# Performance work log

Hardware: AMD Instinct MI355X
Metric: run time of the kernel (lower is better)

## Reference

```python
import jax, jax.numpy as jnp
import numpy as np

N = 40000      # nodes
E = 640000     # edges
G = 2048       # graphs
D = 128        # emb_dim
T = 10         # num_tasks
L = 5          # layers
ATOM_VOCAB = 64
BOND_VOCAB = 8
BN_EPS = 1e-5


def _bn(x, g, b, m, v):
    # inference-mode BatchNorm1d with running stats
    return (x - m) * jax.lax.rsqrt(v + BN_EPS) * g + b


def setup_inputs() -> dict:
    key = jax.random.key(0)
    ks = jax.random.split(key, 24)
    inp = {
        "x_atom": jax.random.randint(ks[0], (N, 9), 0, ATOM_VOCAB),
        "edge_index": jax.random.randint(ks[1], (2, E), 0, N),
        "edge_attr": jax.random.randint(ks[2], (E, 3), 0, BOND_VOCAB),
        "batch": jnp.sort(jax.random.randint(ks[3], (N,), 0, G)),
        # embedding tables
        "atom_emb": jax.random.normal(ks[4], (9, ATOM_VOCAB, D)) * 0.1,
        "bond_emb": jax.random.normal(ks[5], (L, 3, BOND_VOCAB, D)) * 0.1,
        # per-layer GIN params (stacked over L)
        "eps": jnp.zeros((L,)),
        "W1": jax.random.normal(ks[6], (L, D, 2 * D)) * 0.05,
        "b1": jnp.zeros((L, 2 * D)),
        "g1": jnp.ones((L, 2 * D)),
        "bt1": jnp.zeros((L, 2 * D)),
        "m1": jax.random.normal(ks[7], (L, 2 * D)) * 0.1,
        "v1": jax.random.uniform(ks[8], (L, 2 * D), minval=0.5, maxval=1.5),
        "W2": jax.random.normal(ks[9], (L, 2 * D, D)) * 0.05,
        "b2": jnp.zeros((L, D)),
        # outer BatchNorm per layer
        "gO": jnp.ones((L, D)),
        "btO": jnp.zeros((L, D)),
        "mO": jax.random.normal(ks[10], (L, D)) * 0.1,
        "vO": jax.random.uniform(ks[11], (L, D), minval=0.5, maxval=1.5),
        # prediction head
        "Wp": jax.random.normal(ks[12], (D, T)) * 0.05,
        "bp": jnp.zeros((T,)),
    }
    return inp


def reference(x_atom, edge_index, edge_attr, batch, atom_emb, bond_emb, eps,
              W1, b1, g1, bt1, m1, v1, W2, b2, gO, btO, mO, vO, Wp, bp):
    src, dst = edge_index[0], edge_index[1]
    # AtomEncoder: sum of per-feature embeddings -> [N, D]
    x = atom_emb[jnp.arange(9)[None, :], x_atom].sum(axis=1)
    feat3 = jnp.arange(3)[None, :]
    for i in range(L):
        # BondEncoder for this layer -> [E, D]
        e = bond_emb[i][feat3, edge_attr].sum(axis=1)
        # message: relu(x_j + edge_emb); aggregate: scatter-add at dst
        msg = jax.nn.relu(x[src] + e)
        agg = jax.ops.segment_sum(msg, dst, num_segments=N)
        h = (1.0 + eps[i]) * x + agg
        # MLP: Linear -> BN -> ReLU -> Linear
        h = jax.nn.relu(_bn(h @ W1[i] + b1[i], g1[i], bt1[i], m1[i], v1[i]))
        h = h @ W2[i] + b2[i]
        # outer BN; ReLU after all but last layer (dropout = identity in eval)
        x = _bn(h, gO[i], btO[i], mO[i], vO[i])
        if i < L - 1:
            x = jax.nn.relu(x)
    # global mean pool over graphs
    sums = jax.ops.segment_sum(x, batch, num_segments=G)
    cnt = jax.ops.segment_sum(jnp.ones((N,), x.dtype), batch, num_segments=G)
    pooled = sums / jnp.maximum(cnt, 1.0)[:, None]
    return pooled @ Wp + bp
```

## Files before the change

### kernel.cpp

```cpp
#include <hip/hip_runtime.h>
#include <hip/hip_bf16.h>

#define NN 40000
#define NE 640000
#define NG 2048
#define DD 128
#define NT 10
#define NL 5
#define NB 80

typedef __attribute__((ext_vector_type(8))) short short8;
typedef __attribute__((ext_vector_type(4))) float f32x4;
typedef unsigned short ushort_t;

static __device__ __forceinline__ ushort_t f2b(float f) {
    return __bfloat16_as_ushort(__float2bfloat16(f));
}
static __device__ __forceinline__ float b2f(ushort_t u) {
    return __bfloat162float(__ushort_as_bfloat16(u));
}

__global__ void __launch_bounds__(256)
k_setup(const float* __restrict__ W1, const float* __restrict__ W2,
        const float* __restrict__ bemb, const int* __restrict__ xa,
        const float* __restrict__ aemb, const int* __restrict__ ei,
        ushort_t* __restrict__ W1P, ushort_t* __restrict__ W2P,
        ushort_t* __restrict__ ebsum16, ushort_t* __restrict__ x16,
        int* __restrict__ deg) {
    int b = blockIdx.x, t = threadIdx.x;
    if (b < 1280) {
        int tid = b * 256 + t;
        int layer = tid >> 16;
        int r = tid & 65535;
        int half = r >> 15;
        int q = r & 32767;
        int j = q & 7;
        int lane = (q >> 3) & 63;
        if (half == 0) {
            int kk = (q >> 9) & 3;
            int nt = q >> 11;
            int n = nt * 16 + (lane & 15);
            int k = kk * 32 + (lane >> 4) * 8 + j;
            W1P[layer * 32768 + q] = f2b(W1[(layer * DD + k) * 256 + n]);
        } else {
            int kk = (q >> 9) & 7;
            int nt = q >> 12;
            int n = nt * 16 + (lane & 15);
            int k = kk * 32 + (lane >> 4) * 8 + j;
            W2P[layer * 32768 + q] = f2b(W2[(layer * 256 + k) * DD + n]);
        }
        int d = tid & 127;
        int c = (tid >> 7) & 511;
        const float* bl = bemb + (size_t)layer * 3 * 8 * DD;
        ebsum16[tid] = f2b(bl[(c & 7) * DD + d] + bl[(8 + ((c >> 3) & 7)) * DD + d] +
                           bl[(16 + (c >> 6)) * DD + d]);
    } else if (b < 21280) {
        int half = t >> 7, d = t & 127;
        int n = (b - 1280) * 2 + half;
        __shared__ int idx[2][9];
        if (d < 9) idx[half][d] = xa[n * 9 + d];
        __syncthreads();
        float s = 0.f;
#pragma unroll
        for (int f = 0; f < 9; ++f) s += aemb[(f * 64 + idx[half][f]) * DD + d];
        x16[n * DD + d] = f2b(s);
    } else {
        int e = (b - 21280) * 256 + t;
        atomicAdd(&deg[ei[NE + e]], 1);
    }
}


__global__ void k_scan1(const int* __restrict__ deg, int* __restrict__ off,
                        int* __restrict__ blksum) {
    int b = blockIdx.x, t = threadIdx.x;
    int i = b * 256 + t;
    __shared__ int s[256];
    int v = (i < NN) ? deg[i] : 0;
    s[t] = v;
    __syncthreads();
    for (int d = 1; d < 256; d <<= 1) {
        int add = (t >= d) ? s[t - d] : 0;
        __syncthreads();
        s[t] += add;
        __syncthreads();
    }
    if (i <= NN) off[i] = s[t] - v;
    if (t == 255) blksum[b] = s[255];
}

__global__ void k_scan2(int* __restrict__ blk) {
    int t = threadIdx.x;
    __shared__ int s[256];
    int v = blk[t];
    s[t] = v;
    __syncthreads();
    for (int d = 1; d < 256; d <<= 1) {
        int add = (t >= d) ? s[t - d] : 0;
        __syncthreads();
        s[t] += add;
        __syncthreads();
    }
    blk[256 + t] = s[t] - v;
}

__global__ void k_scan3(int* __restrict__ off, const int* __restrict__ blk) {
    int b = blockIdx.x, t = threadIdx.x;
    int i = b * 256 + t;
    if (i <= NN) off[i] += blk[256 + b];
}

__global__ void __launch_bounds__(256)
k_bucket(const int* __restrict__ ei, const int* __restrict__ ea,
         const int* __restrict__ off, int* __restrict__ gbk,
         int2* __restrict__ ebuf) {
    __shared__ int hist[NB];
    __shared__ int sbase[NB];
    int t = threadIdx.x;
    int e0 = blockIdx.x * 1024;
    if (t < NB) hist[t] = 0;
    __syncthreads();
    int rank[4], buck[4], rec[4], dstv[4];
#pragma unroll
    for (int k = 0; k < 4; ++k) {
        int e = e0 + k * 256 + t;
        int src = ei[e];
        int dst = ei[NE + e];
        int a0 = ea[e * 3 + 0], a1 = ea[e * 3 + 1], a2 = ea[e * 3 + 2];
        rec[k] = src | ((a0 | (a1 << 3) | (a2 << 6)) << 16);
        dstv[k] = dst;
        int b = dst >> 9;
        buck[k] = b;
        rank[k] = atomicAdd(&hist[b], 1);
    }
    __syncthreads();
    if (t < NB) sbase[t] = atomicAdd(&gbk[t], hist[t]);
    __syncthreads();
#pragma unroll
    for (int k = 0; k < 4; ++k) {
        int b = buck[k];
        int slot = off[b << 9] + sbase[b] + rank[k];
        ebuf[slot] = make_int2(rec[k], dstv[k]);
    }
}

__global__ void k_scatter2(const int2* __restrict__ ebuf, const int* __restrict__ off,
                           int* __restrict__ cursor, int2* __restrict__ epack) {
    int i = blockIdx.x * 256 + threadIdx.x;
    int2 s = ebuf[i];
    int dst = s.y;
    int p = off[dst] + atomicAdd(&cursor[dst], 1);
    epack[p] = make_int2(s.x & 0xFFFF, s.x >> 16);
}

__global__ void __launch_bounds__(256)
k_gather(const ushort_t* __restrict__ xin, const int* __restrict__ off,
         const int2* __restrict__ epack, const ushort_t* __restrict__ ebsum16,
         const float* __restrict__ eps, int layer, ushort_t* __restrict__ h16) {
    int t = threadIdx.x;
    int lane = t & 63;
    int n = blockIdx.x * 4 + (t >> 6);
    const ushort2* x2 = (const ushort2*)xin;
    const ushort2* eb2 = (const ushort2*)ebsum16;
    ushort2 xv = x2[n * 64 + lane];
    float es = 1.f + eps[layer];
    float ax = es * b2f(xv.x), ay = es * b2f(xv.y);
    int p = off[n], p1 = off[n + 1];

    int2 e0, e1, e2, e3;
    bool have = (p + 4 <= p1);
    if (have) { e0 = epack[p]; e1 = epack[p + 1]; e2 = epack[p + 2]; e3 = epack[p + 3]; }
    while (have) {
        int np = p + 4;
        bool nh = (np + 4 <= p1);
        int2 f0, f1, f2, f3;
        if (nh) { f0 = epack[np]; f1 = epack[np + 1]; f2 = epack[np + 2]; f3 = epack[np + 3]; }
        ushort2 v0 = eb2[e0.y * 64 + lane];
        ushort2 s0 = x2[e0.x * 64 + lane];
        ushort2 v1 = eb2[e1.y * 64 + lane];
        ushort2 s1 = x2[e1.x * 64 + lane];
        ushort2 v2 = eb2[e2.y * 64 + lane];
        ushort2 s2 = x2[e2.x * 64 + lane];
        ushort2 v3 = eb2[e3.y * 64 + lane];
        ushort2 s3 = x2[e3.x * 64 + lane];
        ax += fmaxf(b2f(v0.x) + b2f(s0.x), 0.f) + fmaxf(b2f(v1.x) + b2f(s1.x), 0.f) +
              fmaxf(b2f(v2.x) + b2f(s2.x), 0.f) + fmaxf(b2f(v3.x) + b2f(s3.x), 0.f);
        ay += fmaxf(b2f(v0.y) + b2f(s0.y), 0.f) + fmaxf(b2f(v1.y) + b2f(s1.y), 0.f) +
              fmaxf(b2f(v2.y) + b2f(s2.y), 0.f) + fmaxf(b2f(v3.y) + b2f(s3.y), 0.f);
        p = np;
        e0 = f0; e1 = f1; e2 = f2; e3 = f3;
        have = nh;
    }
    for (; p < p1; ++p) {
        int2 er = epack[p];
        ushort2 ev = eb2[er.y * 64 + lane];
        ushort2 sv = x2[er.x * 64 + lane];
        ax += fmaxf(b2f(ev.x) + b2f(sv.x), 0.f);
        ay += fmaxf(b2f(ev.y) + b2f(sv.y), 0.f);
    }
    ushort2 o;
    o.x = f2b(ax);
    o.y = f2b(ay);
    ((ushort2*)h16)[n * 64 + lane] = o;
}

__global__ void __launch_bounds__(256)
k_mlp_mfma(const ushort_t* __restrict__ h16, const ushort_t* __restrict__ W1P,
           const ushort_t* __restrict__ W2P, const float* __restrict__ b1,
           const float* __restrict__ g1, const float* __restrict__ bt1,
           const float* __restrict__ m1, const float* __restrict__ v1,
           const float* __restrict__ b2_, const float* __restrict__ gO,
           const float* __restrict__ btO, const float* __restrict__ mO,
           const float* __restrict__ vO, int relu, ushort_t* __restrict__ xout) {
    __shared__ ushort_t aS[32 * 136];
    __shared__ ushort_t mid[32 * 264];
    int t = threadIdx.x;
    int wave = t >> 6, lane = t & 63;
    int row0 = blockIdx.x * 32;
    int lrow = lane & 15, quad = lane >> 4;

#pragma unroll
    for (int ps = 0; ps < 2; ++ps) {
        int idx = ps * 256 + t;
        int r = idx >> 4, c = (idx & 15) * 8;
        *(short8*)&aS[r * 136 + c] = *(const short8*)&h16[(row0 + r) * DD + c];
    }
    __syncthreads();

    f32x4 acc1[2][4];
#pragma unroll
    for (int rt = 0; rt < 2; ++rt)
#pragma unroll
        for (int i = 0; i < 4; ++i) acc1[rt][i] = (f32x4){0.f, 0.f, 0.f, 0.f};
#pragma unroll
    for (int kk = 0; kk < 4; ++kk) {
        short8 af0 = *(const short8*)&aS[lrow * 136 + kk * 32 + quad * 8];
        short8 af1 = *(const short8*)&aS[(16 + lrow) * 136 + kk * 32 + quad * 8];
#pragma unroll
        for (int i = 0; i < 4; ++i) {
            int nt = wave * 4 + i;
            short8 bf = *(const short8*)&W1P[((nt * 4 + kk) * 64 + lane) * 8];
            acc1[0][i] = __builtin_amdgcn_mfma_f32_16x16x32_bf16(af0, bf, acc1[0][i], 0, 0, 0);
            acc1[1][i] = __builtin_amdgcn_mfma_f32_16x16x32_bf16(af1, bf, acc1[1][i], 0, 0, 0);
        }
    }
#pragma unroll
    for (int i = 0; i < 4; ++i) {
        int col = (wave * 4 + i) * 16 + lrow;
        float s1 = g1[col] * rsqrtf(v1[col] + 1e-5f);
        float sh = bt1[col] - (m1[col] - b1[col]) * s1;
#pragma unroll
        for (int rt = 0; rt < 2; ++rt)
#pragma unroll
            for (int r = 0; r < 4; ++r) {
                int row = rt * 16 + quad * 4 + r;
                float o = acc1[rt][i][r] * s1 + sh;
                mid[row * 264 + col] = f2b(fmaxf(o, 0.f));
            }
    }
    __syncthreads();

    f32x4 acc2[2][2];
#pragma unroll
    for (int rt = 0; rt < 2; ++rt)
#pragma unroll
        for (int i = 0; i < 2; ++i) acc2[rt][i] = (f32x4){0.f, 0.f, 0.f, 0.f};
#pragma unroll
    for (int kk = 0; kk < 8; ++kk) {
        short8 af0 = *(const short8*)&mid[lrow * 264 + kk * 32 + quad * 8];
        short8 af1 = *(const short8*)&mid[(16 + lrow) * 264 + kk * 32 + quad * 8];
#pragma unroll
        for (int i = 0; i < 2; ++i) {
            int nt = wave * 2 + i;
            short8 bf = *(const short8*)&W2P[((nt * 8 + kk) * 64 + lane) * 8];
            acc2[0][i] = __builtin_amdgcn_mfma_f32_16x16x32_bf16(af0, bf, acc2[0][i], 0, 0, 0);
            acc2[1][i] = __builtin_amdgcn_mfma_f32_16x16x32_bf16(af1, bf, acc2[1][i], 0, 0, 0);
        }
    }
#pragma unroll
    for (int i = 0; i < 2; ++i) {
        int col = (wave * 2 + i) * 16 + lrow;
        float s = gO[col] * rsqrtf(vO[col] + 1e-5f);
        float sh = btO[col] - (mO[col] - b2_[col]) * s;
#pragma unroll
        for (int rt = 0; rt < 2; ++rt)
#pragma unroll
            for (int r = 0; r < 4; ++r) {
                int row = rt * 16 + quad * 4 + r;
                float o = acc2[rt][i][r] * s + sh;
                if (relu) o = fmaxf(o, 0.f);
                xout[(row0 + row) * DD + col] = f2b(o);
            }
    }
}

__global__ void k_poolhead(const ushort_t* __restrict__ x16,
                           const int* __restrict__ batch,
                           const float* __restrict__ Wp, const float* __restrict__ bp,
                           float* __restrict__ out) {
    int g = blockIdx.x, d = threadIdx.x;
    int lo = 0, hi = NN;
    while (lo < hi) { int m = (lo + hi) >> 1; if (batch[m] < g) lo = m + 1; else hi = m; }
    int start = lo;
    hi = NN;
    while (lo < hi) { int m = (lo + hi) >> 1; if (batch[m] < g + 1) lo = m + 1; else hi = m; }
    int end = lo;
    float s = 0.f;
    for (int n = start; n < end; ++n) s += b2f(x16[n * DD + d]);
    float c = fmaxf((float)(end - start), 1.f);
    __shared__ float p[DD];
    p[d] = s / c;
    __syncthreads();
    if (d < NT) {
        float acc = bp[d];
#pragma unroll 8
        for (int k = 0; k < DD; ++k) acc = fmaf(p[k], Wp[k * NT + d], acc);
        out[g * NT + d] = acc;
    }
}

extern "C" void kernel_launch(void* const* d_in, const int* in_sizes, int n_in,
                              void* d_out, int out_size, void* d_ws, size_t ws_size,
                              hipStream_t stream) {
    const int* x_atom = (const int*)d_in[0];
    const int* edge_index = (const int*)d_in[1];
    const int* edge_attr = (const int*)d_in[2];
    const int* batch = (const int*)d_in[3];
    const float* atom_emb = (const float*)d_in[4];
    const float* bond_emb = (const float*)d_in[5];
    const float* eps = (const float*)d_in[6];
    const float* W1 = (const float*)d_in[7];
    const float* b1 = (const float*)d_in[8];
    const float* g1 = (const float*)d_in[9];
    const float* bt1 = (const float*)d_in[10];
    const float* m1 = (const float*)d_in[11];
    const float* v1 = (const float*)d_in[12];
    const float* W2 = (const float*)d_in[13];
    const float* b2 = (const float*)d_in[14];
    const float* gO = (const float*)d_in[15];
    const float* btO = (const float*)d_in[16];
    const float* mO = (const float*)d_in[17];
    const float* vO = (const float*)d_in[18];
    const float* Wp = (const float*)d_in[19];
    const float* bp = (const float*)d_in[20];

    ushort_t* x16a = (ushort_t*)d_ws;
    ushort_t* x16b = x16a + NN * DD;
    ushort_t* h16 = x16b + NN * DD;
    ushort_t* W1P = h16 + NN * DD;
    ushort_t* W2P = W1P + NL * 32768;
    ushort_t* ebsum16 = W2P + NL * 32768;
    int* deg = (int*)(ebsum16 + NL * 65536);
    int* off = deg + NN;
    int* blk = off + 40064;
    int* cursor = blk + 512;
    int* gbk = cursor + NN;
    int2* epack = (int2*)(gbk + 128);
    int2* ebuf = epack + NE;

    hipMemsetAsync(deg, 0, (NN + 40064 + 512 + NN + 128) * sizeof(int), stream);

    k_setup<<<23780, 256, 0, stream>>>(W1, W2, bond_emb, x_atom, atom_emb,
                                       edge_index, W1P, W2P, ebsum16, x16a, deg);
    k_scan1<<<157, 256, 0, stream>>>(deg, off, blk);
    k_scan2<<<1, 256, 0, stream>>>(blk);
    k_scan3<<<157, 256, 0, stream>>>(off, blk);
    k_bucket<<<NE / 1024, 256, 0, stream>>>(edge_index, edge_attr, off, gbk, ebuf);
    k_scatter2<<<NE / 256, 256, 0, stream>>>(ebuf, off, cursor, epack);

    for (int i = 0; i < NL; ++i) {
        ushort_t* xin = (i & 1) ? x16b : x16a;
        ushort_t* xout = (i & 1) ? x16a : x16b;
        k_gather<<<NN / 4, 256, 0, stream>>>(xin, off, epack, ebsum16 + i * 65536,
                                             eps, i, h16);
        k_mlp_mfma<<<NN / 32, 256, 0, stream>>>(
            h16, W1P + (size_t)i * 32768, W2P + (size_t)i * 32768, b1 + i * 256,
            g1 + i * 256, bt1 + i * 256, m1 + i * 256, v1 + i * 256, b2 + i * DD,
            gO + i * DD, btO + i * DD, mO + i * DD, vO + i * DD,
            (i < NL - 1) ? 1 : 0, xout);
    }
    k_poolhead<<<NG, DD, 0, stream>>>(x16b, batch, Wp, bp, (float*)d_out);
}
```

Measured before the change: 427.0 us.

## Fuse neighbor gather into MLP kernel, aggregating directly into shared memory

Merges the per-layer gather kernel and the MFMA MLP kernel into one kernel. Each block's waves aggregate 8 node rows each straight into the shared-memory A tile, removing the intermediate h16 write/read to global memory and one launch per layer. In exchange the gather runs with far fewer blocks and a serial per-wave row loop, which reduces memory-level parallelism for the latency-bound random gathers.

```diff
diff --git a/kernel.cpp b/kernel.cpp
--- a/kernel.cpp
+++ b/kernel.cpp
@@ -154,76 +154,69 @@
 }
 
 __global__ void __launch_bounds__(256)
-k_gather(const ushort_t* __restrict__ xin, const int* __restrict__ off,
-         const int2* __restrict__ epack, const ushort_t* __restrict__ ebsum16,
-         const float* __restrict__ eps, int layer, ushort_t* __restrict__ h16) {
-    int t = threadIdx.x;
-    int lane = t & 63;
-    int n = blockIdx.x * 4 + (t >> 6);
-    const ushort2* x2 = (const ushort2*)xin;
-    const ushort2* eb2 = (const ushort2*)ebsum16;
-    ushort2 xv = x2[n * 64 + lane];
-    float es = 1.f + eps[layer];
-    float ax = es * b2f(xv.x), ay = es * b2f(xv.y);
-    int p = off[n], p1 = off[n + 1];
-
-    int2 e0, e1, e2, e3;
-    bool have = (p + 4 <= p1);
-    if (have) { e0 = epack[p]; e1 = epack[p + 1]; e2 = epack[p + 2]; e3 = epack[p + 3]; }
-    while (have) {
-        int np = p + 4;
-        bool nh = (np + 4 <= p1);
-        int2 f0, f1, f2, f3;
-        if (nh) { f0 = epack[np]; f1 = epack[np + 1]; f2 = epack[np + 2]; f3 = epack[np + 3]; }
-        ushort2 v0 = eb2[e0.y * 64 + lane];
-        ushort2 s0 = x2[e0.x * 64 + lane];
-        ushort2 v1 = eb2[e1.y * 64 + lane];
-        ushort2 s1 = x2[e1.x * 64 + lane];
-        ushort2 v2 = eb2[e2.y * 64 + lane];
-        ushort2 s2 = x2[e2.x * 64 + lane];
-        ushort2 v3 = eb2[e3.y * 64 + lane];
-        ushort2 s3 = x2[e3.x * 64 + lane];
-        ax += fmaxf(b2f(v0.x) + b2f(s0.x), 0.f) + fmaxf(b2f(v1.x) + b2f(s1.x), 0.f) +
-              fmaxf(b2f(v2.x) + b2f(s2.x), 0.f) + fmaxf(b2f(v3.x) + b2f(s3.x), 0.f);
-        ay += fmaxf(b2f(v0.y) + b2f(s0.y), 0.f) + fmaxf(b2f(v1.y) + b2f(s1.y), 0.f) +
-              fmaxf(b2f(v2.y) + b2f(s2.y), 0.f) + fmaxf(b2f(v3.y) + b2f(s3.y), 0.f);
-        p = np;
-        e0 = f0; e1 = f1; e2 = f2; e3 = f3;
-        have = nh;
-    }
-    for (; p < p1; ++p) {
-        int2 er = epack[p];
-        ushort2 ev = eb2[er.y * 64 + lane];
-        ushort2 sv = x2[er.x * 64 + lane];
-        ax += fmaxf(b2f(ev.x) + b2f(sv.x), 0.f);
-        ay += fmaxf(b2f(ev.y) + b2f(sv.y), 0.f);
-    }
-    ushort2 o;
-    o.x = f2b(ax);
-    o.y = f2b(ay);
-    ((ushort2*)h16)[n * 64 + lane] = o;
-}
-
-__global__ void __launch_bounds__(256)
-k_mlp_mfma(const ushort_t* __restrict__ h16, const ushort_t* __restrict__ W1P,
-           const ushort_t* __restrict__ W2P, const float* __restrict__ b1,
-           const float* __restrict__ g1, const float* __restrict__ bt1,
-           const float* __restrict__ m1, const float* __restrict__ v1,
-           const float* __restrict__ b2_, const float* __restrict__ gO,
-           const float* __restrict__ btO, const float* __restrict__ mO,
-           const float* __restrict__ vO, int relu, ushort_t* __restrict__ xout) {
+k_layer(const ushort_t* __restrict__ xin, const int* __restrict__ off,
+        const int2* __restrict__ epack, const ushort_t* __restrict__ ebsum16,
+        const float* __restrict__ eps, int layer,
+        const ushort_t* __restrict__ W1P, const ushort_t* __restrict__ W2P,
+        const float* __restrict__ b1, const float* __restrict__ g1,
+        const float* __restrict__ bt1, const float* __restrict__ m1,
+        const float* __restrict__ v1, const float* __restrict__ b2_,
+        const float* __restrict__ gO, const float* __restrict__ btO,
+        const float* __restrict__ mO, const float* __restrict__ vO,
+        int relu, ushort_t* __restrict__ xout) {
     __shared__ ushort_t aS[32 * 136];
     __shared__ ushort_t mid[32 * 264];
     int t = threadIdx.x;
     int wave = t >> 6, lane = t & 63;
     int row0 = blockIdx.x * 32;
     int lrow = lane & 15, quad = lane >> 4;
-
-#pragma unroll
-    for (int ps = 0; ps < 2; ++ps) {
-        int idx = ps * 256 + t;
-        int r = idx >> 4, c = (idx & 15) * 8;
-        *(short8*)&aS[r * 136 + c] = *(const short8*)&h16[(row0 + r) * DD + c];
+    const ushort2* x2 = (const ushort2*)xin;
+    const ushort2* eb2 = (const ushort2*)ebsum16;
+    float es = 1.f + eps[layer];
+
+#pragma unroll 1
+    for (int rr = 0; rr < 8; ++rr) {
+        int r = (wave << 3) + rr;
+        int n = row0 + r;
+        ushort2 xv = x2[n * 64 + lane];
+        float ax = es * b2f(xv.x), ay = es * b2f(xv.y);
+        int p = off[n], p1 = off[n + 1];
+
+        int2 e0, e1, e2, e3;
+        bool have = (p + 4 <= p1);
+        if (have) { e0 = epack[p]; e1 = epack[p + 1]; e2 = epack[p + 2]; e3 = epack[p + 3]; }
+        while (have) {
+            int np = p + 4;
+            bool nh = (np + 4 <= p1);
+            int2 f0, f1, f2, f3;
+            if (nh) { f0 = epack[np]; f1 = epack[np + 1]; f2 = epack[np + 2]; f3 = epack[np + 3]; }
+            ushort2 v0 = eb2[e0.y * 64 + lane];
+            ushort2 s0 = x2[e0.x * 64 + lane];
+            ushort2 v1 = eb2[e1.y * 64 + lane];
+            ushort2 s1 = x2[e1.x * 64 + lane];
+            ushort2 v2 = eb2[e2.y * 64 + lane];
+            ushort2 s2 = x2[e2.x * 64 + lane];
+            ushort2 v3 = eb2[e3.y * 64 + lane];
+            ushort2 s3 = x2[e3.x * 64 + lane];
+            ax += fmaxf(b2f(v0.x) + b2f(s0.x), 0.f) + fmaxf(b2f(v1.x) + b2f(s1.x), 0.f) +
+                  fmaxf(b2f(v2.x) + b2f(s2.x), 0.f) + fmaxf(b2f(v3.x) + b2f(s3.x), 0.f);
+            ay += fmaxf(b2f(v0.y) + b2f(s0.y), 0.f) + fmaxf(b2f(v1.y) + b2f(s1.y), 0.f) +
+                  fmaxf(b2f(v2.y) + b2f(s2.y), 0.f) + fmaxf(b2f(v3.y) + b2f(s3.y), 0.f);
+            p = np;
+            e0 = f0; e1 = f1; e2 = f2; e3 = f3;
+            have = nh;
+        }
+        for (; p < p1; ++p) {
+            int2 er = epack[p];
+            ushort2 ev = eb2[er.y * 64 + lane];
+            ushort2 sv = x2[er.x * 64 + lane];
+            ax += fmaxf(b2f(ev.x) + b2f(sv.x), 0.f);
+            ay += fmaxf(b2f(ev.y) + b2f(sv.y), 0.f);
+        }
+        ushort2 o;
+        o.x = f2b(ax);
+        o.y = f2b(ay);
+        *(ushort2*)&aS[r * 136 + lane * 2] = o;
     }
     __syncthreads();
 
@@ -371,10 +364,9 @@
     for (int i = 0; i < NL; ++i) {
         ushort_t* xin = (i & 1) ? x16b : x16a;
         ushort_t* xout = (i & 1) ? x16a : x16b;
-        k_gather<<<NN / 4, 256, 0, stream>>>(xin, off, epack, ebsum16 + i * 65536,
-                                             eps, i, h16);
-        k_mlp_mfma<<<NN / 32, 256, 0, stream>>>(
-            h16, W1P + (size_t)i * 32768, W2P + (size_t)i * 32768, b1 + i * 256,
+        k_layer<<<NN / 32, 256, 0, stream>>>(
+            xin, off, epack, ebsum16 + i * 65536, eps, i,
+            W1P + (size_t)i * 32768, W2P + (size_t)i * 32768, b1 + i * 256,
             g1 + i * 256, bt1 + i * 256, m1 + i * 256, v1 + i * 256, b2 + i * DD,
             gO + i * DD, btO + i * DD, mO + i * DD, vO + i * DD,
             (i < NL - 1) ? 1 : 0, xout);
```

Measured after the change: 532.1 us. 24.6% more time.
